# Performance work log

Measured on AMD Instinct MI355X. Metric: run time of the kernel, lower is better.

The kernel has to match this reference:

```python
import jax, jax.numpy as jnp
import numpy as np
import math

B, N, D, H = 32, 577, 768, 12
HD = D // H  # 64
WS = 24  # window size
NUM_REL_DIST = (2 * WS - 1) * (2 * WS - 1) + 3  # 2212


def _build_rel_pos_index():
    ch, cw = np.arange(WS), np.arange(WS)
    coords = np.stack(np.meshgrid(ch, cw, indexing='ij'))  # [2, WS, WS]
    cf = coords.reshape(2, -1)  # [2, WS*WS]
    rel = cf[:, :, None] - cf[:, None, :]  # [2, WS*WS, WS*WS]
    rel = rel.transpose(1, 2, 0).astype(np.int64)
    rel[:, :, 0] += WS - 1
    rel[:, :, 1] += WS - 1
    rel[:, :, 0] *= 2 * WS - 1
    idx = np.zeros((WS * WS + 1, WS * WS + 1), dtype=np.int64)
    idx[1:, 1:] = rel.sum(-1)
    idx[0, 0:] = NUM_REL_DIST - 3
    idx[0:, 0] = NUM_REL_DIST - 2
    idx[0, 0] = NUM_REL_DIST - 1
    return idx.astype(np.int32)


def setup_inputs() -> dict:
    key = jax.random.key(0)
    ks = jax.random.split(key, 7)
    s = 1.0 / math.sqrt(D)
    return {
        'hidden_states': jax.random.normal(ks[0], (B, N, D), jnp.float32),
        'q_w': jax.random.normal(ks[1], (D, D), jnp.float32) * s,
        'q_b': jax.random.normal(ks[2], (D,), jnp.float32) * 0.02,
        'k_w': jax.random.normal(ks[3], (D, D), jnp.float32) * s,
        'v_w': jax.random.normal(ks[4], (D, D), jnp.float32) * s,
        'v_b': jax.random.normal(ks[5], (D,), jnp.float32) * 0.02,
        'rel_pos_table': jax.random.normal(ks[6], (NUM_REL_DIST, H), jnp.float32) * 0.02,
        'rel_pos_index': jnp.asarray(_build_rel_pos_index()),
    }


def reference(hidden_states, q_w, q_b, k_w, v_w, v_b, rel_pos_table, rel_pos_index):
    # QKV projections (torch Linear: x @ W.T + b); key has no bias
    q = hidden_states @ q_w.T + q_b  # [B,N,D]
    k = hidden_states @ k_w.T        # [B,N,D]
    v = hidden_states @ v_w.T + v_b  # [B,N,D]

    def heads(x):
        return x.reshape(B, N, H, HD).transpose(0, 2, 1, 3)  # [B,H,N,HD]

    q, k, v = heads(q), heads(k), heads(v)
    scores = jnp.einsum('bhqd,bhkd->bhqk', q, k) / math.sqrt(HD)
    # relative position bias: table lookup -> [N,N,H] -> [H,N,N]
    bias = rel_pos_table[rel_pos_index.reshape(-1)].reshape(N, N, H)
    scores = scores + bias.transpose(2, 0, 1)[None]
    probs = jax.nn.softmax(scores, axis=-1)  # dropout p=0 (eval)
    ctx = jnp.einsum('bhqk,bhkd->bhqd', probs, v)
    return ctx.transpose(0, 2, 1, 3).reshape(B, N, D)
```

## Files before the change

kernel.cpp:

```cpp
#include <hip/hip_runtime.h>
#include <hip/hip_bf16.h>

#define B_  32
#define N_  577
#define D_  768
#define H_  12
#define HD_ 64
#define M_  (B_ * N_)
#define NW_ (3 * D_)
#define VN_ 640
#define BPAD_ 640
#define SCALE_ 0.18033688f

typedef __bf16 bf16_t;
typedef __bf16 bf16x8 __attribute__((ext_vector_type(8)));
typedef __bf16 bf16x4 __attribute__((ext_vector_type(4)));
typedef float  f32x4  __attribute__((ext_vector_type(4)));

static __device__ __forceinline__ bf16x8 ldg8(const bf16_t* p) {
    return *reinterpret_cast<const bf16x8*>(p);
}

#define GLOAD_LDS16(g, l)                                                     \
    __builtin_amdgcn_global_load_lds(                                         \
        (const __attribute__((address_space(1))) void*)(g),                   \
        (__attribute__((address_space(3))) void*)(l), 16, 0, 0)

__global__ void cvt_f32_bf16(const float* __restrict__ src,
                             bf16_t* __restrict__ dst, int n4) {
    int i = blockIdx.x * blockDim.x + threadIdx.x;
    if (i < n4) {
        float4 f = reinterpret_cast<const float4*>(src)[i];
        bf16x4 o;
        o.x = (bf16_t)f.x; o.y = (bf16_t)f.y; o.z = (bf16_t)f.z; o.w = (bf16_t)f.w;
        *reinterpret_cast<bf16x4*>(dst + (size_t)i * 4) = o;
    }
}

__global__ void cvt3_f32_bf16(const float* __restrict__ s0,
                              const float* __restrict__ s1,
                              const float* __restrict__ s2,
                              bf16_t* __restrict__ dst, int n4) {
    int i = blockIdx.x * blockDim.x + threadIdx.x;
    if (i < n4) {
        const float* src = blockIdx.y == 0 ? s0 : (blockIdx.y == 1 ? s1 : s2);
        float4 f = reinterpret_cast<const float4*>(src)[i];
        bf16x4 o;
        o.x = (bf16_t)f.x; o.y = (bf16_t)f.y; o.z = (bf16_t)f.z; o.w = (bf16_t)f.w;
        *reinterpret_cast<bf16x4*>(dst + (size_t)blockIdx.y * n4 * 4 + (size_t)i * 4) = o;
    }
}

__global__ void build_bias_t(const float* __restrict__ table,
                             const int* __restrict__ idx,
                             float* __restrict__ biasT) {
    int col = blockIdx.x;
    if (col < N_) {
        for (int row = threadIdx.x; row < BPAD_; row += blockDim.x) {
            int rr = row < N_ ? row : (N_ - 1);
            int id = idx[rr * N_ + col];
            const float* trow = table + (size_t)id * H_;
#pragma unroll
            for (int h = 0; h < H_; ++h)
                biasT[((size_t)h * BPAD_ + col) * BPAD_ + row] =
                    trow[h] * 1.44269504f;
        }
    } else {
        for (int row = threadIdx.x; row < BPAD_; row += blockDim.x) {
#pragma unroll
            for (int h = 0; h < H_; ++h)
                biasT[((size_t)h * BPAD_ + col) * BPAD_ + row] = -1e30f;
        }
    }
}

__global__ __launch_bounds__(256) void qkv_gemm(
    const bf16_t* __restrict__ hb, const bf16_t* __restrict__ W,
    const float* __restrict__ qb, const float* __restrict__ vb,
    bf16_t* __restrict__ Q, bf16_t* __restrict__ K, bf16_t* __restrict__ VT)
{
    __shared__ __align__(16) char lds[65536];

    int tid = threadIdx.x;
    int w  = tid >> 6, l = tid & 63;
    int lr = l & 15, lg = l >> 4;
    int wm = w & 1,  wn = w >> 1;

    int wg = blockIdx.x;
    int xcd = wg & 7, pos = wg >> 3;
    const int Q8 = 2610 / 8, R8 = 2610 % 8;
    int base = xcd < R8 ? xcd * (Q8 + 1) : R8 * (Q8 + 1) + (xcd - R8) * Q8;
    int wgid = base + pos;
    int bx = wgid / 18, y = wgid - bx * 18;
    int brow = bx * 128;
    int mat = y / 6, ysub = y - mat * 6;
    int cbase = ysub * 128;

    int srow = tid >> 3;
    int sslot = (tid & 7) ^ (srow & 7);
    const bf16_t* pa[4];
    const bf16_t* pb[4];
#pragma unroll
    for (int r = 0; r < 4; ++r) {
        int ra = brow + r * 32 + srow; ra = ra < M_ ? ra : (M_ - 1);
        pa[r] = hb + (size_t)ra * D_ + sslot * 8;
        pb[r] = W + (size_t)(y * 128 + r * 32 + srow) * D_ + sslot * 8;
    }

    auto stage = [&](int buf, int k) {
#pragma unroll
        for (int r = 0; r < 4; ++r) {
            GLOAD_LDS16(pa[r] + k, lds + buf * 16384 + r * 4096 + tid * 16);
            GLOAD_LDS16(pb[r] + k, lds + 32768 + buf * 16384 + r * 4096 + tid * 16);
        }
    };

    f32x4 acc[4][4] = {};
    stage(0, 0);
    int cur = 0;
    for (int t = 0; t < 12; ++t) {
        if (t < 11) {
            stage(cur ^ 1, (t + 1) * 64);
            asm volatile("s_waitcnt vmcnt(8)" ::: "memory");
        } else {
            asm volatile("s_waitcnt vmcnt(0)" ::: "memory");
        }
        __builtin_amdgcn_s_barrier();
        __builtin_amdgcn_sched_barrier(0);

        const char* pA = lds + cur * 16384;
        const char* pB = lds + 32768 + cur * 16384;
#pragma unroll
        for (int kk = 0; kk < 2; ++kk) {
            bf16x8 af[4];
#pragma unroll
            for (int m = 0; m < 4; ++m) {
                int row = wm * 64 + m * 16 + lr;
                af[m] = *reinterpret_cast<const bf16x8*>(
                    pA + row * 128 + (((kk * 4 + lg) ^ (lr & 7)) << 4));
            }
#pragma unroll
            for (int n = 0; n < 4; ++n) {
                int row = wn * 64 + n * 16 + lr;
                bf16x8 bfr = *reinterpret_cast<const bf16x8*>(
                    pB + row * 128 + (((kk * 4 + lg) ^ (lr & 7)) << 4));
#pragma unroll
                for (int m = 0; m < 4; ++m)
                    acc[m][n] = __builtin_amdgcn_mfma_f32_16x16x32_bf16(
                        af[m], bfr, acc[m][n], 0, 0, 0);
            }
        }
        __builtin_amdgcn_sched_barrier(0);
        __builtin_amdgcn_s_barrier();
        cur ^= 1;
    }

    bf16_t* ep = (bf16_t*)lds;
    if (mat < 2) {
#pragma unroll
        for (int m = 0; m < 4; ++m)
#pragma unroll
            for (int n = 0; n < 4; ++n) {
                int col = wn * 64 + n * 16 + lr;
#pragma unroll
                for (int j = 0; j < 4; ++j) {
                    int row = wm * 64 + m * 16 + lg * 4 + j;
                    float v = acc[m][n][j];
                    v = (mat == 0) ? (v + qb[cbase + col]) * SCALE_ : v;
                    ep[row * 132 + col] = (bf16_t)v;
                }
            }
        __syncthreads();
        bf16_t* dst0 = (mat == 0) ? Q : K;
#pragma unroll
        for (int k = 0; k < 8; ++k) {
            int c = k * 256 + tid;
            int row = c >> 4, cc = c & 15;
            int grow = brow + row;
            if (grow < M_) {
                int bb = grow / N_, nn = grow - bb * N_;
                int col0 = cc * 8;
                int hh = ysub * 2 + (col0 >> 6);
                int hd0 = col0 & 63;
                bf16x8 vc = *reinterpret_cast<const bf16x8*>(ep + row * 132 + col0);
                *reinterpret_cast<bf16x8*>(
                    dst0 + ((size_t)(bb * H_ + hh) * N_ + nn) * HD_ + hd0) = vc;
            }
        }
    } else {
#pragma unroll
        for (int m = 0; m < 4; ++m)
#pragma unroll
            for (int n = 0; n < 4; ++n) {
                int col = wn * 64 + n * 16 + lr;
                float badd = vb[cbase + col];
#pragma unroll
                for (int j = 0; j < 4; ++j) {
                    int row = wm * 64 + m * 16 + lg * 4 + j;
                    ep[col * 132 + row] = (bf16_t)(acc[m][n][j] + badd);
                }
            }
        __syncthreads();
#pragma unroll
        for (int k = 0; k < 8; ++k) {
            int c = k * 256 + tid;
            int col = c >> 4, rc = c & 15;
            int grow0 = brow + rc * 8;
            int hh = ysub * 2 + (col >> 6), hd = col & 63;
            int bb = grow0 / N_, nn0 = grow0 - bb * N_;
            if (nn0 + 8 <= N_ && grow0 + 8 <= M_) {
                *reinterpret_cast<bf16x8*>(
                    VT + ((size_t)(bb * H_ + hh) * HD_ + hd) * VN_ + nn0) =
                    *reinterpret_cast<const bf16x8*>(ep + col * 132 + rc * 8);
            } else {
                for (int jj = 0; jj < 8; ++jj) {
                    int grow = grow0 + jj;
                    if (grow >= M_) break;
                    int b2 = grow / N_, n2 = grow - b2 * N_;
                    VT[((size_t)(b2 * H_ + hh) * HD_ + hd) * VN_ + n2] =
                        ep[col * 132 + rc * 8 + jj];
                }
            }
        }
    }
}

__global__ __launch_bounds__(256) void attn(
    const bf16_t* __restrict__ Q, const bf16_t* __restrict__ K,
    const bf16_t* __restrict__ VT, const float* __restrict__ biasT,
    float* __restrict__ out)
{
    __shared__ __align__(16) char Kl[2][8192];
    __shared__ __align__(16) char Vl[2][8192];
    __shared__ __align__(16) char Pl[4][2048];

    int tid = threadIdx.x;
    int w = tid >> 6, l = tid & 63, lr = l & 15, lg = l >> 4;

    int wg = blockIdx.x;
    int wgid = (wg & 7) * 480 + (wg >> 3);
    int h = wgid / 320;
    int rem = wgid - h * 320;
    int b = rem / 10;
    int qt = rem - b * 10;

    const bf16_t* Qp = Q  + (size_t)(b * H_ + h) * N_ * HD_;
    const bf16_t* Kp = K  + (size_t)(b * H_ + h) * N_ * HD_;
    const bf16_t* Vp = VT + (size_t)(b * H_ + h) * HD_ * VN_;
    const float*  bp = biasT + (size_t)h * BPAD_ * BPAD_;

    int q0 = qt * 64 + w * 16;
    int qrow = q0 + lr;
    int qrow_c = qrow < N_ ? qrow : (N_ - 1);
    bf16x8 aQ0 = ldg8(Qp + (size_t)qrow_c * HD_ + lg * 8);
    bf16x8 aQ1 = ldg8(Qp + (size_t)qrow_c * HD_ + 32 + lg * 8);

    bf16x8 vone;
#pragma unroll
    for (int i = 0; i < 8; ++i) vone[i] = (bf16_t)1.0f;

    int rloc = l >> 3;
    int cswz = (l & 7) ^ rloc;
    const bf16_t* Kst[2];
    const bf16_t* Vst[2];
#pragma unroll
    for (int rnd = 0; rnd < 2; ++rnd) {
        int r = rnd * 32 + w * 8 + rloc;
        Kst[rnd] = Kp + (size_t)r * HD_ + cswz * 8;
        Vst[rnd] = Vp + (size_t)r * VN_ + cswz * 8;
    }

    f32x4 o[4] = {};
    f32x4 osum = {};
    char* Pw = Pl[w];
    const int NT = 10;

    auto stageKV = [&](int buf, int k0) {
#pragma unroll
        for (int rnd = 0; rnd < 2; ++rnd)
            GLOAD_LDS16(Kst[rnd] + (size_t)k0 * HD_,
                        Kl[buf] + rnd * 4096 + w * 1024);
#pragma unroll
        for (int rnd = 0; rnd < 2; ++rnd)
            GLOAD_LDS16(Vst[rnd] + k0, Vl[buf] + rnd * 4096 + w * 1024);
    };
    auto loadBias = [&](int k0, f32x4* bbv) {
#pragma unroll
        for (int kt = 0; kt < 4; ++kt)
            bbv[kt] = *reinterpret_cast<const f32x4*>(
                bp + (size_t)(k0 + kt * 16 + lr) * BPAD_ + q0 + lg * 4);
    };

    auto tile = [&](int t, int rbuf, const f32x4* bbcur, f32x4* bbnxt) {
        int k0 = t * 64;
        if (t + 1 < NT) {
            stageKV(rbuf ^ 1, k0 + 64);
            loadBias(k0 + 64, bbnxt);
        }
        __builtin_amdgcn_sched_barrier(0);

        f32x4 s[4];
        __builtin_amdgcn_s_setprio(1);
#pragma unroll
        for (int kt = 0; kt < 4; ++kt) {
            int r = kt * 16 + lr;
            bf16x8 kf0 = *reinterpret_cast<const bf16x8*>(
                Kl[rbuf] + r * 128 + ((lg ^ (r & 7)) << 4));
            bf16x8 kf1 = *reinterpret_cast<const bf16x8*>(
                Kl[rbuf] + r * 128 + (((4 + lg) ^ (r & 7)) << 4));
            f32x4 a = __builtin_amdgcn_mfma_f32_16x16x32_bf16(
                aQ0, kf0, bbcur[kt], 0, 0, 0);
            s[kt] = __builtin_amdgcn_mfma_f32_16x16x32_bf16(aQ1, kf1, a, 0, 0, 0);
        }
        __builtin_amdgcn_s_setprio(0);

#pragma unroll
        for (int kt = 0; kt < 4; ++kt)
#pragma unroll
            for (int j = 0; j < 4; ++j) {
                float p = __builtin_amdgcn_exp2f(s[kt][j]);
                int row = lg * 4 + j;
                int byte = (row * 128 + (kt * 16 + lr) * 2) ^ ((row & 7) << 4);
                *reinterpret_cast<bf16_t*>(Pw + byte) = (bf16_t)p;
            }

        __builtin_amdgcn_s_setprio(1);
#pragma unroll
        for (int kc = 0; kc < 2; ++kc) {
            int pbyte = (lr * 128 + kc * 64 + lg * 16) ^ ((lr & 7) << 4);
            bf16x8 aP = *reinterpret_cast<const bf16x8*>(Pw + pbyte);
            osum = __builtin_amdgcn_mfma_f32_16x16x32_bf16(aP, vone, osum, 0, 0, 0);
#pragma unroll
            for (int ft = 0; ft < 4; ++ft) {
                int d = ft * 16 + lr;
                bf16x8 bV = *reinterpret_cast<const bf16x8*>(
                    Vl[rbuf] + d * 128 + (((kc * 4 + lg) ^ (d & 7)) << 4));
                o[ft] = __builtin_amdgcn_mfma_f32_16x16x32_bf16(aP, bV, o[ft], 0, 0, 0);
            }
        }
        __builtin_amdgcn_s_setprio(0);
        __builtin_amdgcn_sched_barrier(0);

        if (t + 1 < NT) asm volatile("s_waitcnt vmcnt(4)" ::: "memory");
        else            asm volatile("s_waitcnt vmcnt(0)" ::: "memory");
        __builtin_amdgcn_s_barrier();
        __builtin_amdgcn_sched_barrier(0);
    };

    f32x4 bbA[4], bbB[4];
    stageKV(0, 0);
    loadBias(0, bbA);
    asm volatile("s_waitcnt vmcnt(4)" ::: "memory");
    __builtin_amdgcn_s_barrier();
    __builtin_amdgcn_sched_barrier(0);

    for (int tp = 0; tp < NT / 2; ++tp) {
        tile(tp * 2,     0, bbA, bbB);
        tile(tp * 2 + 1, 1, bbB, bbA);
    }

#pragma unroll
    for (int j = 0; j < 4; ++j) {
        int row = q0 + lg * 4 + j;
        if (row < N_) {
            float inv = 1.f / osum[j];
#pragma unroll
            for (int ft = 0; ft < 4; ++ft)
                out[((size_t)(b * N_ + row)) * D_ + h * HD_ + ft * 16 + lr] =
                    o[ft][j] * inv;
        }
    }
}

extern "C" void kernel_launch(void* const* d_in, const int* in_sizes, int n_in,
                              void* d_out, int out_size, void* d_ws, size_t ws_size,
                              hipStream_t stream)
{
    const float* hs    = (const float*)d_in[0];
    const float* q_w   = (const float*)d_in[1];
    const float* q_b   = (const float*)d_in[2];
    const float* k_w   = (const float*)d_in[3];
    const float* v_w   = (const float*)d_in[4];
    const float* v_b   = (const float*)d_in[5];
    const float* table = (const float*)d_in[6];
    const int*   rpi   = (const int*)d_in[7];
    float* out = (float*)d_out;

    char* ws = (char*)d_ws;
    size_t off = 0;
    auto alloc = [&](size_t bytes) {
        char* p = ws + off;
        off = (off + bytes + 255) & ~(size_t)255;
        return p;
    };
    bf16_t* hb  = (bf16_t*)alloc((size_t)M_ * D_ * 2);
    bf16_t* Wc  = (bf16_t*)alloc((size_t)NW_ * D_ * 2);
    bf16_t* Qb  = (bf16_t*)alloc((size_t)B_ * H_ * N_ * HD_ * 2);
    bf16_t* Kb  = (bf16_t*)alloc((size_t)B_ * H_ * N_ * HD_ * 2 + 16384);
    bf16_t* VTb = (bf16_t*)alloc((size_t)B_ * H_ * HD_ * VN_ * 2);
    float*  bia = (float*)alloc((size_t)H_ * BPAD_ * BPAD_ * 4);

    int n4h = M_ * D_ / 4;
    cvt_f32_bf16<<<(n4h + 255) / 256, 256, 0, stream>>>(hs, hb, n4h);
    int n4w = D_ * D_ / 4;
    cvt3_f32_bf16<<<dim3((n4w + 255) / 256, 3), 256, 0, stream>>>(
        q_w, k_w, v_w, Wc, n4w);
    build_bias_t<<<BPAD_, 256, 0, stream>>>(table, rpi, bia);

    qkv_gemm<<<2610, 256, 0, stream>>>(hb, Wc, q_b, v_b, Qb, Kb, VTb);

    attn<<<3840, 256, 0, stream>>>(Qb, Kb, VTb, bia, out);
}
```

Baseline: 218.8 us.

## Keep softmax probabilities in registers via transposed QK MFMA and permuted keys

```diff
diff --git a/kernel.cpp b/kernel.cpp
--- a/kernel.cpp
+++ b/kernel.cpp
@@ -20,6 +20,9 @@
 static __device__ __forceinline__ bf16x8 ldg8(const bf16_t* p) {
     return *reinterpret_cast<const bf16x8*>(p);
 }
+
+#define GPERM(r) (((r) & 32) | (((r) & 8) << 1) | (((r) & 4) << 1) | \
+                  (((r) & 16) >> 2) | ((r) & 3))
 
 #define GLOAD_LDS16(g, l)                                                     \
     __builtin_amdgcn_global_load_lds(                                         \
@@ -51,25 +54,25 @@
     }
 }
 
-__global__ void build_bias_t(const float* __restrict__ table,
-                             const int* __restrict__ idx,
-                             float* __restrict__ biasT) {
-    int col = blockIdx.x;
-    if (col < N_) {
-        for (int row = threadIdx.x; row < BPAD_; row += blockDim.x) {
-            int rr = row < N_ ? row : (N_ - 1);
-            int id = idx[rr * N_ + col];
+__global__ void build_bias2(const float* __restrict__ table,
+                            const int* __restrict__ idx,
+                            float* __restrict__ bias2) {
+    int q = blockIdx.x;
+    int rr = q < N_ ? q : (N_ - 1);
+    for (int kl = threadIdx.x; kl < BPAD_; kl += blockDim.x) {
+        int s = kl & 63;
+        int gk = (kl & ~63) | GPERM(s);
+        if (gk < N_) {
+            int id = idx[rr * N_ + gk];
             const float* trow = table + (size_t)id * H_;
 #pragma unroll
             for (int h = 0; h < H_; ++h)
-                biasT[((size_t)h * BPAD_ + col) * BPAD_ + row] =
+                bias2[((size_t)h * BPAD_ + q) * BPAD_ + kl] =
                     trow[h] * 1.44269504f;
-        }
-    } else {
-        for (int row = threadIdx.x; row < BPAD_; row += blockDim.x) {
+        } else {
 #pragma unroll
             for (int h = 0; h < H_; ++h)
-                biasT[((size_t)h * BPAD_ + col) * BPAD_ + row] = -1e30f;
+                bias2[((size_t)h * BPAD_ + q) * BPAD_ + kl] = -1e30f;
         }
     }
 }
@@ -227,12 +230,11 @@
 
 __global__ __launch_bounds__(256) void attn(
     const bf16_t* __restrict__ Q, const bf16_t* __restrict__ K,
-    const bf16_t* __restrict__ VT, const float* __restrict__ biasT,
+    const bf16_t* __restrict__ VT, const float* __restrict__ bias2,
     float* __restrict__ out)
 {
     __shared__ __align__(16) char Kl[2][8192];
     __shared__ __align__(16) char Vl[2][8192];
-    __shared__ __align__(16) char Pl[4][2048];
 
     int tid = threadIdx.x;
     int w = tid >> 6, l = tid & 63, lr = l & 15, lg = l >> 4;
@@ -247,7 +249,7 @@
     const bf16_t* Qp = Q  + (size_t)(b * H_ + h) * N_ * HD_;
     const bf16_t* Kp = K  + (size_t)(b * H_ + h) * N_ * HD_;
     const bf16_t* Vp = VT + (size_t)(b * H_ + h) * HD_ * VN_;
-    const float*  bp = biasT + (size_t)h * BPAD_ * BPAD_;
+    const float*  bp = bias2 + (size_t)h * BPAD_ * BPAD_;
 
     int q0 = qt * 64 + w * 16;
     int qrow = q0 + lr;
@@ -266,13 +268,13 @@
 #pragma unroll
     for (int rnd = 0; rnd < 2; ++rnd) {
         int r = rnd * 32 + w * 8 + rloc;
-        Kst[rnd] = Kp + (size_t)r * HD_ + cswz * 8;
+        int gk = GPERM(r);
+        Kst[rnd] = Kp + (size_t)gk * HD_ + cswz * 8;
         Vst[rnd] = Vp + (size_t)r * VN_ + cswz * 8;
     }
 
     f32x4 o[4] = {};
     f32x4 osum = {};
-    char* Pw = Pl[w];
     const int NT = 10;
 
     auto stageKV = [&](int buf, int k0) {
@@ -285,10 +287,10 @@
             GLOAD_LDS16(Vst[rnd] + k0, Vl[buf] + rnd * 4096 + w * 1024);
     };
     auto loadBias = [&](int k0, f32x4* bbv) {
+        const float* brow = bp + (size_t)(q0 + lr) * BPAD_ + k0;
 #pragma unroll
         for (int kt = 0; kt < 4; ++kt)
-            bbv[kt] = *reinterpret_cast<const f32x4*>(
-                bp + (size_t)(k0 + kt * 16 + lr) * BPAD_ + q0 + lg * 4);
+            bbv[kt] = *reinterpret_cast<const f32x4*>(brow + kt * 16 + lg * 4);
     };
 
     auto tile = [&](int t, int rbuf, const f32x4* bbcur, f32x4* bbnxt) {
@@ -309,26 +311,30 @@
             bf16x8 kf1 = *reinterpret_cast<const bf16x8*>(
                 Kl[rbuf] + r * 128 + (((4 + lg) ^ (r & 7)) << 4));
             f32x4 a = __builtin_amdgcn_mfma_f32_16x16x32_bf16(
-                aQ0, kf0, bbcur[kt], 0, 0, 0);
-            s[kt] = __builtin_amdgcn_mfma_f32_16x16x32_bf16(aQ1, kf1, a, 0, 0, 0);
+                kf0, aQ0, bbcur[kt], 0, 0, 0);
+            s[kt] = __builtin_amdgcn_mfma_f32_16x16x32_bf16(kf1, aQ1, a, 0, 0, 0);
         }
         __builtin_amdgcn_s_setprio(0);
 
+        float p[4][4];
 #pragma unroll
         for (int kt = 0; kt < 4; ++kt)
 #pragma unroll
-            for (int j = 0; j < 4; ++j) {
-                float p = __builtin_amdgcn_exp2f(s[kt][j]);
-                int row = lg * 4 + j;
-                int byte = (row * 128 + (kt * 16 + lr) * 2) ^ ((row & 7) << 4);
-                *reinterpret_cast<bf16_t*>(Pw + byte) = (bf16_t)p;
-            }
+            for (int j = 0; j < 4; ++j)
+                p[kt][j] = __builtin_amdgcn_exp2f(s[kt][j]);
 
         __builtin_amdgcn_s_setprio(1);
 #pragma unroll
         for (int kc = 0; kc < 2; ++kc) {
-            int pbyte = (lr * 128 + kc * 64 + lg * 16) ^ ((lr & 7) << 4);
-            bf16x8 aP = *reinterpret_cast<const bf16x8*>(Pw + pbyte);
+            bf16x8 aP;
+            aP[0] = (bf16_t)p[2 * kc][0];
+            aP[1] = (bf16_t)p[2 * kc][1];
+            aP[2] = (bf16_t)p[2 * kc][2];
+            aP[3] = (bf16_t)p[2 * kc][3];
+            aP[4] = (bf16_t)p[2 * kc + 1][0];
+            aP[5] = (bf16_t)p[2 * kc + 1][1];
+            aP[6] = (bf16_t)p[2 * kc + 1][2];
+            aP[7] = (bf16_t)p[2 * kc + 1][3];
             osum = __builtin_amdgcn_mfma_f32_16x16x32_bf16(aP, vone, osum, 0, 0, 0);
 #pragma unroll
             for (int ft = 0; ft < 4; ++ft) {
@@ -405,7 +411,7 @@
     int n4w = D_ * D_ / 4;
     cvt3_f32_bf16<<<dim3((n4w + 255) / 256, 3), 256, 0, stream>>>(
         q_w, k_w, v_w, Wc, n4w);
-    build_bias_t<<<BPAD_, 256, 0, stream>>>(table, rpi, bia);
+    build_bias2<<<BPAD_, 256, 0, stream>>>(table, rpi, bia);
 
     qkv_gemm<<<2610, 256, 0, stream>>>(hb, Wc, q_b, v_b, Qb, Kb, VTb);
 
```

Result: faster. 214.1 us, median of 2 (-2.1%).
